# Optimization experiments

Hardware: AMD Instinct MI355X
Metric: run time of the kernel (lower is better)

## Reference

```python
import jax, jax.numpy as jnp
import numpy as np

N_NODES = 100000
N_EDGES = 600000
N_ETYPES = 4
IN_DIM = 128
OUT_DIM = 128
N_STEPS = 8
N_GRAPHS = 128


def setup_inputs() -> dict:
    key = jax.random.key(0)
    ks = jax.random.split(key, 12)
    features = jax.random.normal(ks[0], (N_NODES, IN_DIM), dtype=jnp.float32)
    edge_src = jax.random.randint(ks[1], (N_EDGES,), 0, N_NODES, dtype=jnp.int32)
    edge_dst = jax.random.randint(ks[2], (N_EDGES,), 0, N_NODES, dtype=jnp.int32)
    edge_types = jax.random.randint(ks[3], (N_EDGES,), 0, N_ETYPES, dtype=jnp.int32)
    graph_ids = jnp.sort(jax.random.randint(ks[4], (N_NODES,), 0, N_GRAPHS, dtype=jnp.int32))
    s = 1.0 / np.sqrt(OUT_DIM)
    W_edge = jax.random.uniform(ks[5], (N_ETYPES, OUT_DIM, OUT_DIM), jnp.float32, -s, s)
    W_ih = jax.random.uniform(ks[6], (3 * OUT_DIM, OUT_DIM), jnp.float32, -s, s)
    W_hh = jax.random.uniform(ks[7], (3 * OUT_DIM, OUT_DIM), jnp.float32, -s, s)
    b_ih = jax.random.uniform(ks[8], (3 * OUT_DIM,), jnp.float32, -s, s)
    b_hh = jax.random.uniform(ks[9], (3 * OUT_DIM,), jnp.float32, -s, s)
    W_cls = jax.random.uniform(ks[10], (1, OUT_DIM), jnp.float32, -s, s)
    b_cls = jax.random.uniform(ks[11], (1,), jnp.float32, -s, s)
    return dict(features=features, edge_src=edge_src, edge_dst=edge_dst,
                edge_types=edge_types, graph_ids=graph_ids, W_edge=W_edge,
                W_ih=W_ih, W_hh=W_hh, b_ih=b_ih, b_hh=b_hh, W_cls=W_cls, b_cls=b_cls)


def _gru_cell(x, h, W_ih, W_hh, b_ih, b_hh):
    gi = x @ W_ih.T + b_ih  # [N, 3*out]
    gh = h @ W_hh.T + b_hh
    i_r, i_z, i_n = jnp.split(gi, 3, axis=-1)
    h_r, h_z, h_n = jnp.split(gh, 3, axis=-1)
    r = jax.nn.sigmoid(i_r + h_r)
    z = jax.nn.sigmoid(i_z + h_z)
    n = jnp.tanh(i_n + r * h_n)
    return (1.0 - z) * n + z * h


def reference(features, edge_src, edge_dst, edge_types, graph_ids,
              W_edge, W_ih, W_hh, b_ih, b_hh, W_cls, b_cls):
    n_nodes = features.shape[0]
    out_dim = W_edge.shape[-1]
    # DGL GatedGraphConv zero-pads features to out_feats
    pad = out_dim - features.shape[1]
    h = jnp.pad(features, ((0, 0), (0, pad))) if pad > 0 else features

    def step(h, _):
        # per-edge-type linear transform of all nodes: [etype, N, out]
        ht = jnp.einsum('nd,edh->enh', h, W_edge)
        m = ht[edge_types, edge_src]  # gather per-edge messages [E, out]
        a = jax.ops.segment_sum(m, edge_dst, num_segments=n_nodes)
        return _gru_cell(a, h, W_ih, W_hh, b_ih, b_hh), None

    h, _ = jax.lax.scan(step, h, None, length=N_STEPS)
    # de-batchify + sum over nodes per graph == segment_sum over graph ids
    pooled = jax.ops.segment_sum(h, graph_ids, num_segments=N_GRAPHS)  # [B, out]
    logits = pooled @ W_cls.T + b_cls  # [B, 1]
    return jax.nn.sigmoid(logits).squeeze(-1)  # [B]
```

## Files before the change

### kernel.cpp

```cpp
#include <hip/hip_runtime.h>
#include <cstdint>

#define NNODES 100000
#define NEDGES 600000
#define NETYPES 4
#define DIM 128
#define NSTEPS 8
#define NGRAPHS 128
#define NBINS (NETYPES * NNODES)
#define SCAN_BLK 391
#define NTILES (NNODES / 32)
#define PGRID 512

typedef short s16x8 __attribute__((ext_vector_type(8)));
typedef float f32x4 __attribute__((ext_vector_type(4)));

#define MFMA(a, b, c) __builtin_amdgcn_mfma_f32_16x16x32_bf16(a, b, c, 0, 0, 0)

static __device__ inline unsigned short f2bf(float x) {
  unsigned int u = __float_as_uint(x);
  unsigned int r = (u + 0x7FFFu + ((u >> 16) & 1u)) >> 16;
  return (unsigned short)r;
}
static __device__ inline float bf2f(unsigned short b) {
  return __uint_as_float(((unsigned int)b) << 16);
}

__global__ __launch_bounds__(128) void fill_kernel(float* __restrict__ out, int n, float v) {
  int i = blockIdx.x * 128 + threadIdx.x;
  if (i < n) out[i] = v;
}

__global__ __launch_bounds__(256) void cvt_h_kernel(const float* __restrict__ f,
                                                    unsigned short* __restrict__ h, int n4) {
  int i = blockIdx.x * 256 + threadIdx.x;
  if (i < n4) {
    float4 v = ((const float4*)f)[i];
    ushort4 u = {f2bf(v.x), f2bf(v.y), f2bf(v.z), f2bf(v.w)};
    ((ushort4*)h)[i] = u;
  }
}

__global__ __launch_bounds__(256) void cvt_we_kernel(const float* __restrict__ W,
                                                     unsigned short* __restrict__ WT) {
  int i = blockIdx.x * 256 + threadIdx.x;
  if (i < NETYPES * DIM * DIM) {
    int e = i >> 14;
    int r = i & 16383;
    int d = r >> 7;
    int j = r & 127;
    WT[(e << 14) + (j << 7) + d] = f2bf(W[i]);
  }
}

__global__ __launch_bounds__(256) void cvt_w_kernel(const float* __restrict__ W,
                                                    unsigned short* __restrict__ Wb, int n) {
  int i = blockIdx.x * 256 + threadIdx.x;
  if (i < n) Wb[i] = f2bf(W[i]);
}

__global__ __launch_bounds__(256) void hist_kernel(const int* __restrict__ edst,
                                                   const int* __restrict__ etyp,
                                                   int* __restrict__ bins) {
  int e = blockIdx.x * 256 + threadIdx.x;
  if (e < NEDGES) atomicAdd(&bins[etyp[e] * NNODES + edst[e]], 1);
}

__global__ __launch_bounds__(256) void scan1_kernel(const int* __restrict__ bins,
                                                    int* __restrict__ rp,
                                                    int* __restrict__ bsum) {
  __shared__ int sh[256];
  int b = blockIdx.x, t = threadIdx.x;
  int base = b * 1024 + t * 4;
  int v0 = 0, v1 = 0, v2 = 0, v3 = 0;
  if (base + 3 < NBINS) {
    int4 q = *(const int4*)(bins + base);
    v0 = q.x; v1 = q.y; v2 = q.z; v3 = q.w;
  } else {
    if (base < NBINS) v0 = bins[base];
    if (base + 1 < NBINS) v1 = bins[base + 1];
    if (base + 2 < NBINS) v2 = bins[base + 2];
  }
  int s = v0 + v1 + v2 + v3;
  sh[t] = s;
  __syncthreads();
  for (int off = 1; off < 256; off <<= 1) {
    int x = (t >= off) ? sh[t - off] : 0;
    __syncthreads();
    if (t >= off) sh[t] += x;
    __syncthreads();
  }
  int run = sh[t] - s;
  if (t == 255) bsum[b] = sh[255];
  if (base < NBINS) rp[base] = run;
  run += v0;
  if (base + 1 < NBINS) rp[base + 1] = run;
  run += v1;
  if (base + 2 < NBINS) rp[base + 2] = run;
  run += v2;
  if (base + 3 < NBINS) rp[base + 3] = run;
}

__global__ __launch_bounds__(512) void scan2_kernel(const int* __restrict__ bsum,
                                                    int* __restrict__ boffs,
                                                    int* __restrict__ rp) {
  __shared__ int sh[512];
  int t = threadIdx.x;
  int v = (t < SCAN_BLK) ? bsum[t] : 0;
  sh[t] = v;
  __syncthreads();
  for (int off = 1; off < 512; off <<= 1) {
    int x = (t >= off) ? sh[t - off] : 0;
    __syncthreads();
    if (t >= off) sh[t] += x;
    __syncthreads();
  }
  if (t < SCAN_BLK) boffs[t] = sh[t] - v;
  if (t == SCAN_BLK - 1) rp[NBINS] = sh[t];
}

__global__ __launch_bounds__(256) void scan3_kernel(int* __restrict__ rp,
                                                    const int* __restrict__ boffs) {
  int b = blockIdx.x, t = threadIdx.x;
  int base = b * 1024 + t * 4;
  int off = boffs[b];
#pragma unroll
  for (int i = 0; i < 4; ++i)
    if (base + i < NBINS) rp[base + i] += off;
}

__global__ __launch_bounds__(256) void fill_edges_kernel(const int* __restrict__ esrc,
                                                         const int* __restrict__ edst,
                                                         const int* __restrict__ etyp,
                                                         int* __restrict__ cursor,
                                                         int* __restrict__ esrc_s) {
  int e = blockIdx.x * 256 + threadIdx.x;
  if (e < NEDGES) {
    int slot = atomicAdd(&cursor[etyp[e] * NNODES + edst[e]], 1);
    esrc_s[slot] = esrc[e];
  }
}

__global__ __launch_bounds__(256) void agg4_kernel(const unsigned short* __restrict__ hbf,
                                                   const int* __restrict__ rp,
                                                   const int* __restrict__ esrc_s,
                                                   unsigned short* __restrict__ agg4) {
  int w = (blockIdx.x * 256 + threadIdx.x) >> 6;
  int lane = threadIdx.x & 63;
  if (w >= NNODES) return;
#pragma unroll
  for (int ty = 0; ty < NETYPES; ++ty) {
    int beg = rp[ty * NNODES + w];
    int end = rp[ty * NNODES + w + 1];
    float ax = 0.f, ay = 0.f;
    for (int e = beg; e < end; ++e) {
      int s = esrc_s[e];
      ushort2 u = *(const ushort2*)(hbf + (size_t)s * DIM + lane * 2);
      ax += bf2f(u.x);
      ay += bf2f(u.y);
    }
    unsigned int packed = ((unsigned int)f2bf(ay) << 16) | (unsigned int)f2bf(ax);
    *(unsigned int*)(agg4 + (size_t)ty * NNODES * DIM + (size_t)w * DIM + lane * 2) = packed;
  }
}

__global__ __launch_bounds__(512, 2) void transform_kernel(const unsigned short* __restrict__ agg4,
                                                           const unsigned short* __restrict__ WeT,
                                                           unsigned short* __restrict__ abf) {
  __shared__ s16x8 lds[2][2048];
  const int t = threadIdx.x;
  const int wid = t >> 6, lane = t & 63;
  const int l15 = lane & 15, kg = lane >> 4;
  const int j0 = wid * 16, jb = j0 + kg * 4;

  s16x8 wf[4][4];
#pragma unroll
  for (int ty = 0; ty < 4; ++ty)
#pragma unroll
    for (int c = 0; c < 4; ++c)
      wf[ty][c] = *(const s16x8*)(WeT + (ty << 14) + ((j0 + l15) << 7) + c * 32 + kg * 8);

  int chk[4], lby[4];
#pragma unroll
  for (int i = 0; i < 4; ++i) {
    chk[i] = t + i * 512;
    int row = (chk[i] & 511) >> 4;
    int w16 = chk[i] & 15;
    lby[i] = (chk[i] >> 9) * 8192 + row * 256 + ((w16 ^ (row & 7)) << 4);
  }
  auto gsrc = [&](int i, int tile) -> const s16x8* {
    int ty = chk[i] >> 9;
    int row = (chk[i] & 511) >> 4;
    int w16 = chk[i] & 15;
    return (const s16x8*)(agg4 + (size_t)ty * NNODES * DIM +
                          (size_t)(tile * 32 + row) * DIM + w16 * 8);
  };

  int tile = blockIdx.x;
  if (tile >= NTILES) return;
  s16x8 st[4];
#pragma unroll
  for (int i = 0; i < 4; ++i) st[i] = *gsrc(i, tile);
#pragma unroll
  for (int i = 0; i < 4; ++i) *(s16x8*)((char*)&lds[0][0] + lby[i]) = st[i];
  int nx = tile + gridDim.x;
  bool hasnx = nx < NTILES;
  if (hasnx)
#pragma unroll
    for (int i = 0; i < 4; ++i) st[i] = *gsrc(i, nx);
  __syncthreads();
  int cur = 0;

  while (true) {
    if (hasnx) {
#pragma unroll
      for (int i = 0; i < 4; ++i) *(s16x8*)((char*)&lds[cur ^ 1][0] + lby[i]) = st[i];
    }
    int nx2 = nx + gridDim.x;
    bool has2 = hasnx && (nx2 < NTILES);
    if (has2) {
#pragma unroll
      for (int i = 0; i < 4; ++i) st[i] = *gsrc(i, nx2);
    }

    f32x4 acc[2] = {(f32x4){0.f, 0.f, 0.f, 0.f}, (f32x4){0.f, 0.f, 0.f, 0.f}};
    char* B0 = (char*)&lds[cur][0];
#pragma unroll
    for (int ty = 0; ty < 4; ++ty) {
#pragma unroll
      for (int c = 0; c < 4; ++c) {
        s16x8 afr[2];
#pragma unroll
        for (int nb = 0; nb < 2; ++nb) {
          int row = nb * 16 + l15;
          afr[nb] = *(const s16x8*)(B0 + ty * 8192 + row * 256 +
                                    ((c * 64 + kg * 16) ^ ((row & 7) << 4)));
        }
        acc[0] = MFMA(wf[ty][c], afr[0], acc[0]);
        acc[1] = MFMA(wf[ty][c], afr[1], acc[1]);
      }
    }
    const int n0 = tile * 32;
#pragma unroll
    for (int nb = 0; nb < 2; ++nb) {
      int n = n0 + nb * 16 + l15;
      ushort4 u = {f2bf(acc[nb][0]), f2bf(acc[nb][1]), f2bf(acc[nb][2]), f2bf(acc[nb][3])};
      *(ushort4*)(abf + (size_t)n * DIM + jb) = u;
    }
    __syncthreads();
    if (!hasnx) break;
    tile = nx;
    nx = nx2;
    hasnx = has2;
    cur ^= 1;
  }
}

__global__ __launch_bounds__(512, 2) void gru_mfma_kernel(const unsigned short* __restrict__ abf,
                                                          unsigned short* __restrict__ hbf,
                                                          const unsigned short* __restrict__ Wih,
                                                          const unsigned short* __restrict__ Whh,
                                                          const float* __restrict__ b_ih,
                                                          const float* __restrict__ b_hh) {
  __shared__ s16x8 lds[2][1024];
  const int t = threadIdx.x;
  const int wid = t >> 6, lane = t & 63;
  const int l15 = lane & 15, kg = lane >> 4;
  const int j0 = wid * 16, jb = j0 + kg * 4;

  s16x8 wI[3][4], wH[3][4];
#pragma unroll
  for (int g = 0; g < 3; ++g)
#pragma unroll
    for (int c = 0; c < 4; ++c) {
      int jrow = g * 128 + j0 + l15;
      wI[g][c] = *(const s16x8*)(Wih + (jrow << 7) + c * 32 + kg * 8);
      wH[g][c] = *(const s16x8*)(Whh + (jrow << 7) + c * 32 + kg * 8);
    }
  float4 bir = *(const float4*)(b_ih + jb);
  float4 biz = *(const float4*)(b_ih + 128 + jb);
  float4 bin_ = *(const float4*)(b_ih + 256 + jb);
  float4 bhr = *(const float4*)(b_hh + jb);
  float4 bhz = *(const float4*)(b_hh + 128 + jb);
  float4 bhn = *(const float4*)(b_hh + 256 + jb);

  int chk0 = t, chk1 = t + 512;
  int row0 = (chk0 & 511) >> 4, w160 = chk0 & 15;
  int row1 = (chk1 & 511) >> 4, w161 = chk1 & 15;
  int lb0 = (chk0 >> 9) * 8192 + row0 * 256 + ((w160 ^ (row0 & 7)) << 4);
  int lb1 = (chk1 >> 9) * 8192 + row1 * 256 + ((w161 ^ (row1 & 7)) << 4);
  int hbyte_lo = (jb * 2) & 15;
  int hbyte_slot = (jb * 2) >> 4;

  int tile = blockIdx.x;
  if (tile >= NTILES) return;
  s16x8 st0, st1;
  st0 = *(const s16x8*)(((chk0 >> 9) ? hbf : abf) + (size_t)(tile * 32 + row0) * DIM + w160 * 8);
  st1 = *(const s16x8*)(((chk1 >> 9) ? hbf : abf) + (size_t)(tile * 32 + row1) * DIM + w161 * 8);
  *(s16x8*)((char*)&lds[0][0] + lb0) = st0;
  *(s16x8*)((char*)&lds[0][0] + lb1) = st1;
  int nx = tile + gridDim.x;
  bool hasnx = nx < NTILES;
  if (hasnx) {
    st0 = *(const s16x8*)(((chk0 >> 9) ? hbf : abf) + (size_t)(nx * 32 + row0) * DIM + w160 * 8);
    st1 = *(const s16x8*)(((chk1 >> 9) ? hbf : abf) + (size_t)(nx * 32 + row1) * DIM + w161 * 8);
  }
  __syncthreads();
  int cur = 0;

  while (true) {
    if (hasnx) {
      *(s16x8*)((char*)&lds[cur ^ 1][0] + lb0) = st0;
      *(s16x8*)((char*)&lds[cur ^ 1][0] + lb1) = st1;
    }
    int nx2 = nx + gridDim.x;
    bool has2 = hasnx && (nx2 < NTILES);
    if (has2) {
      st0 = *(const s16x8*)(((chk0 >> 9) ? hbf : abf) + (size_t)(nx2 * 32 + row0) * DIM + w160 * 8);
      st1 = *(const s16x8*)(((chk1 >> 9) ? hbf : abf) + (size_t)(nx2 * 32 + row1) * DIM + w161 * 8);
    }

    f32x4 gi[3][2], gh[3][2];
#pragma unroll
    for (int g = 0; g < 3; ++g)
#pragma unroll
      for (int nb = 0; nb < 2; ++nb) {
        gi[g][nb] = (f32x4){0.f, 0.f, 0.f, 0.f};
        gh[g][nb] = (f32x4){0.f, 0.f, 0.f, 0.f};
      }
    char* aB = (char*)&lds[cur][0];
    char* hB = aB + 8192;
#pragma unroll
    for (int c = 0; c < 4; ++c) {
      s16x8 afr[2], hfr[2];
#pragma unroll
      for (int nb = 0; nb < 2; ++nb) {
        int row = nb * 16 + l15;
        int off = row * 256 + ((c * 64 + kg * 16) ^ ((row & 7) << 4));
        afr[nb] = *(const s16x8*)(aB + off);
        hfr[nb] = *(const s16x8*)(hB + off);
      }
#pragma unroll
      for (int g = 0; g < 3; ++g) {
        gi[g][0] = MFMA(wI[g][c], afr[0], gi[g][0]);
        gi[g][1] = MFMA(wI[g][c], afr[1], gi[g][1]);
        gh[g][0] = MFMA(wH[g][c], hfr[0], gh[g][0]);
        gh[g][1] = MFMA(wH[g][c], hfr[1], gh[g][1]);
      }
    }

    const int n0 = tile * 32;
#pragma unroll
    for (int nb = 0; nb < 2; ++nb) {
      int row = nb * 16 + l15;
      int n = n0 + row;
      int hb = row * 256 + ((hbyte_slot << 4) ^ ((row & 7) << 4)) + hbyte_lo;
      ushort4 hold4 = *(const ushort4*)(hB + hb);
      ushort4 outu;
#pragma unroll
      for (int reg = 0; reg < 4; ++reg) {
        float ir = gi[0][nb][reg] + ((const float*)&bir)[reg];
        float iz = gi[1][nb][reg] + ((const float*)&biz)[reg];
        float in_ = gi[2][nb][reg] + ((const float*)&bin_)[reg];
        float hr = gh[0][nb][reg] + ((const float*)&bhr)[reg];
        float hz = gh[1][nb][reg] + ((const float*)&bhz)[reg];
        float hn = gh[2][nb][reg] + ((const float*)&bhn)[reg];
        float r = 1.f / (1.f + __expf(-(ir + hr)));
        float z = 1.f / (1.f + __expf(-(iz + hz)));
        float x = in_ + r * hn;
        float ex = __expf(2.f * x);
        float nn = 1.f - 2.f / (ex + 1.f);
        float ho = bf2f(((const unsigned short*)&hold4)[reg]);
        float hv = (1.f - z) * nn + z * ho;
        ((unsigned short*)&outu)[reg] = f2bf(hv);
      }
      *(ushort4*)(hbf + (size_t)n * DIM + jb) = outu;
    }
    __syncthreads();
    if (!hasnx) break;
    tile = nx;
    nx = nx2;
    hasnx = has2;
    cur ^= 1;
  }
}

__global__ __launch_bounds__(128) void pool_kernel(const unsigned short* __restrict__ h,
                                                   const int* __restrict__ gid,
                                                   float* __restrict__ pooled) {
  int j = threadIdx.x;
  int n0 = blockIdx.x * 32;
  int end = n0 + 32;
  if (end > NNODES) end = NNODES;
  int cur = gid[n0];
  float acc = 0.f;
  for (int n = n0; n < end; ++n) {
    int g = gid[n];
    if (g != cur) {
      atomicAdd(&pooled[cur * DIM + j], acc);
      acc = 0.f;
      cur = g;
    }
    acc += bf2f(h[(size_t)n * DIM + j]);
  }
  atomicAdd(&pooled[cur * DIM + j], acc);
}

__global__ __launch_bounds__(128) void cls_kernel(const float* __restrict__ pooled,
                                                  const float* __restrict__ Wc,
                                                  const float* __restrict__ bc,
                                                  float* __restrict__ out) {
  int g = threadIdx.x;
  float acc = bc[0];
  for (int k = 0; k < DIM; ++k) acc = fmaf(pooled[g * DIM + k], Wc[k], acc);
  out[g] = 1.f / (1.f + __expf(-acc));
}

extern "C" void kernel_launch(void* const* d_in, const int* in_sizes, int n_in,
                              void* d_out, int out_size, void* d_ws, size_t ws_size,
                              hipStream_t stream) {
  const float* features = (const float*)d_in[0];
  const int* esrc = (const int*)d_in[1];
  const int* edst = (const int*)d_in[2];
  const int* etyp = (const int*)d_in[3];
  const int* gids = (const int*)d_in[4];
  const float* W_edge = (const float*)d_in[5];
  const float* W_ih = (const float*)d_in[6];
  const float* W_hh = (const float*)d_in[7];
  const float* b_ih = (const float*)d_in[8];
  const float* b_hh = (const float*)d_in[9];
  const float* W_cls = (const float*)d_in[10];
  const float* b_cls = (const float*)d_in[11];
  float* out = (float*)d_out;

  const size_t nd = (size_t)NNODES * DIM;
  char* p = (char*)d_ws;
  auto take = [&](size_t bytes) {
    char* q = p;
    p += (bytes + 15) & ~(size_t)15;
    return (void*)q;
  };
  unsigned short* agg4 = (unsigned short*)take(NETYPES * nd * 2);
  unsigned short* abf = (unsigned short*)take(nd * 2);
  unsigned short* hbf = (unsigned short*)take(nd * 2);
  unsigned short* WeT = (unsigned short*)take(NETYPES * DIM * DIM * 2);
  unsigned short* Wihb = (unsigned short*)take(384 * DIM * 2);
  unsigned short* Whhb = (unsigned short*)take(384 * DIM * 2);
  int* rp = (int*)take((NBINS + 1) * 4);
  int* cursor = (int*)take(NBINS * 4);
  int* bsum = (int*)take(512 * 4);
  int* boffs = (int*)take(512 * 4);
  int* esrc_s = (int*)take(NEDGES * 4);
  float* pooled = (float*)take(NGRAPHS * DIM * 4);
  size_t need = (size_t)(p - (char*)d_ws);

  if (ws_size < need) {
    fill_kernel<<<(out_size + 127) / 128, 128, 0, stream>>>(out, out_size, 0.5f);
    return;
  }

  cvt_h_kernel<<<(int)(nd / 4 + 255) / 256, 256, 0, stream>>>(features, hbf, (int)(nd / 4));
  cvt_we_kernel<<<(NETYPES * DIM * DIM + 255) / 256, 256, 0, stream>>>(W_edge, WeT);
  cvt_w_kernel<<<(384 * DIM + 255) / 256, 256, 0, stream>>>(W_ih, Wihb, 384 * DIM);
  cvt_w_kernel<<<(384 * DIM + 255) / 256, 256, 0, stream>>>(W_hh, Whhb, 384 * DIM);

  hipMemsetAsync(cursor, 0, (size_t)NBINS * 4, stream);
  hist_kernel<<<(NEDGES + 255) / 256, 256, 0, stream>>>(edst, etyp, cursor);
  scan1_kernel<<<SCAN_BLK, 256, 0, stream>>>(cursor, rp, bsum);
  scan2_kernel<<<1, 512, 0, stream>>>(bsum, boffs, rp);
  scan3_kernel<<<SCAN_BLK, 256, 0, stream>>>(rp, boffs);
  hipMemcpyAsync(cursor, rp, (size_t)NBINS * 4, hipMemcpyDeviceToDevice, stream);
  fill_edges_kernel<<<(NEDGES + 255) / 256, 256, 0, stream>>>(esrc, edst, etyp, cursor, esrc_s);

  for (int s = 0; s < NSTEPS; ++s) {
    agg4_kernel<<<(NNODES * 64 + 255) / 256, 256, 0, stream>>>(hbf, rp, esrc_s, agg4);
    transform_kernel<<<PGRID, 512, 0, stream>>>(agg4, WeT, abf);
    gru_mfma_kernel<<<PGRID, 512, 0, stream>>>(abf, hbf, Wihb, Whhb, b_ih, b_hh);
  }

  hipMemsetAsync(pooled, 0, (size_t)NGRAPHS * DIM * 4, stream);
  pool_kernel<<<(NNODES + 31) / 32, 128, 0, stream>>>(hbf, gids, pooled);
  cls_kernel<<<1, 128, 0, stream>>>(pooled, W_cls, b_cls, out);
}
```

Baseline: 1.355 ms.

## Fuse per-type edge aggregation into MFMA transform kernel via shared memory

```diff
diff --git a/kernel.cpp b/kernel.cpp
--- a/kernel.cpp
+++ b/kernel.cpp
@@ -141,33 +141,12 @@
   }
 }
 
-__global__ __launch_bounds__(256) void agg4_kernel(const unsigned short* __restrict__ hbf,
-                                                   const int* __restrict__ rp,
-                                                   const int* __restrict__ esrc_s,
-                                                   unsigned short* __restrict__ agg4) {
-  int w = (blockIdx.x * 256 + threadIdx.x) >> 6;
-  int lane = threadIdx.x & 63;
-  if (w >= NNODES) return;
-#pragma unroll
-  for (int ty = 0; ty < NETYPES; ++ty) {
-    int beg = rp[ty * NNODES + w];
-    int end = rp[ty * NNODES + w + 1];
-    float ax = 0.f, ay = 0.f;
-    for (int e = beg; e < end; ++e) {
-      int s = esrc_s[e];
-      ushort2 u = *(const ushort2*)(hbf + (size_t)s * DIM + lane * 2);
-      ax += bf2f(u.x);
-      ay += bf2f(u.y);
-    }
-    unsigned int packed = ((unsigned int)f2bf(ay) << 16) | (unsigned int)f2bf(ax);
-    *(unsigned int*)(agg4 + (size_t)ty * NNODES * DIM + (size_t)w * DIM + lane * 2) = packed;
-  }
-}
-
-__global__ __launch_bounds__(512, 2) void transform_kernel(const unsigned short* __restrict__ agg4,
-                                                           const unsigned short* __restrict__ WeT,
-                                                           unsigned short* __restrict__ abf) {
-  __shared__ s16x8 lds[2][2048];
+__global__ __launch_bounds__(512, 4) void msg_kernel(const unsigned short* __restrict__ hbf,
+                                                     const int* __restrict__ rp,
+                                                     const int* __restrict__ esrc_s,
+                                                     const unsigned short* __restrict__ WeT,
+                                                     unsigned short* __restrict__ abf) {
+  __shared__ char lds[32768];
   const int t = threadIdx.x;
   const int wid = t >> 6, lane = t & 63;
   const int l15 = lane & 15, kg = lane >> 4;
@@ -180,51 +159,34 @@
     for (int c = 0; c < 4; ++c)
       wf[ty][c] = *(const s16x8*)(WeT + (ty << 14) + ((j0 + l15) << 7) + c * 32 + kg * 8);
 
-  int chk[4], lby[4];
-#pragma unroll
-  for (int i = 0; i < 4; ++i) {
-    chk[i] = t + i * 512;
-    int row = (chk[i] & 511) >> 4;
-    int w16 = chk[i] & 15;
-    lby[i] = (chk[i] >> 9) * 8192 + row * 256 + ((w16 ^ (row & 7)) << 4);
-  }
-  auto gsrc = [&](int i, int tile) -> const s16x8* {
-    int ty = chk[i] >> 9;
-    int row = (chk[i] & 511) >> 4;
-    int w16 = chk[i] & 15;
-    return (const s16x8*)(agg4 + (size_t)ty * NNODES * DIM +
-                          (size_t)(tile * 32 + row) * DIM + w16 * 8);
-  };
-
-  int tile = blockIdx.x;
-  if (tile >= NTILES) return;
-  s16x8 st[4];
-#pragma unroll
-  for (int i = 0; i < 4; ++i) st[i] = *gsrc(i, tile);
-#pragma unroll
-  for (int i = 0; i < 4; ++i) *(s16x8*)((char*)&lds[0][0] + lby[i]) = st[i];
-  int nx = tile + gridDim.x;
-  bool hasnx = nx < NTILES;
-  if (hasnx)
-#pragma unroll
-    for (int i = 0; i < 4; ++i) st[i] = *gsrc(i, nx);
-  __syncthreads();
-  int cur = 0;
-
-  while (true) {
-    if (hasnx) {
-#pragma unroll
-      for (int i = 0; i < 4; ++i) *(s16x8*)((char*)&lds[cur ^ 1][0] + lby[i]) = st[i];
-    }
-    int nx2 = nx + gridDim.x;
-    bool has2 = hasnx && (nx2 < NTILES);
-    if (has2) {
-#pragma unroll
-      for (int i = 0; i < 4; ++i) st[i] = *gsrc(i, nx2);
-    }
+  const int swz_w = lane >> 2;
+  const int sub = (lane & 3) * 4;
+
+  for (int tile = blockIdx.x; tile < NTILES; tile += gridDim.x) {
+    const int n0 = tile * 32;
+#pragma unroll
+    for (int i = 0; i < 4; ++i) {
+      int row = wid * 4 + i;
+      int node = n0 + row;
+      int lbase = row * 256 + ((swz_w ^ (row & 7)) << 4) + sub;
+#pragma unroll
+      for (int ty = 0; ty < 4; ++ty) {
+        int idx = ty * NNODES + node;
+        int beg = rp[idx], end = rp[idx + 1];
+        float ax = 0.f, ay = 0.f;
+        for (int e = beg; e < end; ++e) {
+          int s = esrc_s[e];
+          ushort2 u = *(const ushort2*)(hbf + (size_t)s * DIM + lane * 2);
+          ax += bf2f(u.x);
+          ay += bf2f(u.y);
+        }
+        unsigned int packed = ((unsigned int)f2bf(ay) << 16) | (unsigned int)f2bf(ax);
+        *(unsigned int*)(lds + ty * 8192 + lbase) = packed;
+      }
+    }
+    __syncthreads();
 
     f32x4 acc[2] = {(f32x4){0.f, 0.f, 0.f, 0.f}, (f32x4){0.f, 0.f, 0.f, 0.f}};
-    char* B0 = (char*)&lds[cur][0];
 #pragma unroll
     for (int ty = 0; ty < 4; ++ty) {
 #pragma unroll
@@ -233,14 +195,13 @@
 #pragma unroll
         for (int nb = 0; nb < 2; ++nb) {
           int row = nb * 16 + l15;
-          afr[nb] = *(const s16x8*)(B0 + ty * 8192 + row * 256 +
+          afr[nb] = *(const s16x8*)(lds + ty * 8192 + row * 256 +
                                     ((c * 64 + kg * 16) ^ ((row & 7) << 4)));
         }
         acc[0] = MFMA(wf[ty][c], afr[0], acc[0]);
         acc[1] = MFMA(wf[ty][c], afr[1], acc[1]);
       }
     }
-    const int n0 = tile * 32;
 #pragma unroll
     for (int nb = 0; nb < 2; ++nb) {
       int n = n0 + nb * 16 + l15;
@@ -248,11 +209,6 @@
       *(ushort4*)(abf + (size_t)n * DIM + jb) = u;
     }
     __syncthreads();
-    if (!hasnx) break;
-    tile = nx;
-    nx = nx2;
-    hasnx = has2;
-    cur ^= 1;
   }
 }
 
@@ -440,7 +396,6 @@
     p += (bytes + 15) & ~(size_t)15;
     return (void*)q;
   };
-  unsigned short* agg4 = (unsigned short*)take(NETYPES * nd * 2);
   unsigned short* abf = (unsigned short*)take(nd * 2);
   unsigned short* hbf = (unsigned short*)take(nd * 2);
   unsigned short* WeT = (unsigned short*)take(NETYPES * DIM * DIM * 2);
@@ -473,8 +428,7 @@
   fill_edges_kernel<<<(NEDGES + 255) / 256, 256, 0, stream>>>(esrc, edst, etyp, cursor, esrc_s);
 
   for (int s = 0; s < NSTEPS; ++s) {
-    agg4_kernel<<<(NNODES * 64 + 255) / 256, 256, 0, stream>>>(hbf, rp, esrc_s, agg4);
-    transform_kernel<<<PGRID, 512, 0, stream>>>(agg4, WeT, abf);
+    msg_kernel<<<PGRID, 512, 0, stream>>>(hbf, rp, esrc_s, WeT, abf);
     gru_mfma_kernel<<<PGRID, 512, 0, stream>>>(abf, hbf, Wihb, Whhb, b_ih, b_hh);
   }
 
```

New measurement: 1.768 ms. +30.5%, slower.
